# Kernel optimization log

Hardware: AMD Instinct MI355X
Metric: run time of the kernel (lower is better)

The kernel has to match this reference:

```python
import jax, jax.numpy as jnp
import numpy as np

B, S, D, DM, H = 2, 2048, 1024, 1024, 16
DH = D // H
EPS = 1e-5


def layernorm(x, g, b):
    m = jnp.mean(x, axis=-1, keepdims=True)
    v = jnp.mean(jnp.square(x - m), axis=-1, keepdims=True)
    return (x - m) * jax.lax.rsqrt(v + EPS) * g + b


def setup_inputs() -> dict:
    key = jax.random.key(0)
    ks = jax.random.split(key, 16)
    std = 0.02
    p = {
        'x': jax.random.normal(ks[0], (B, S, D), jnp.float32),
        'h': jnp.zeros((B, DM), jnp.float32),
        'c': jnp.zeros((B, DM), jnp.float32),
        'Wq': jax.random.normal(ks[1], (D, D), jnp.float32) * std,
        'Wk': jax.random.normal(ks[2], (D, D), jnp.float32) * std,
        'Wv': jax.random.normal(ks[3], (D, D), jnp.float32) * std,
        'Wo': jax.random.normal(ks[4], (D, D), jnp.float32) * std,
        'Wmk': jax.random.normal(ks[5], (DM, D), jnp.float32) * std,
        'Wmv': jax.random.normal(ks[6], (DM, D), jnp.float32) * std,
        'Wih': jax.random.normal(ks[7], (D, 4 * DM), jnp.float32) * std,
        'Whh': jax.random.normal(ks[8], (DM, 4 * DM), jnp.float32) * std,
        'b_ih': jnp.zeros((4 * DM,), jnp.float32),
        'b_hh': jnp.zeros((4 * DM,), jnp.float32),
        'W1': jax.random.normal(ks[9], (D, 4 * D), jnp.float32) * std,
        'bf1': jnp.zeros((4 * D,), jnp.float32),
        'W2': jax.random.normal(ks[10], (4 * D, D), jnp.float32) * std,
        'bf2': jnp.zeros((D,), jnp.float32),
        'g1': jnp.ones((D,), jnp.float32), 'be1': jnp.zeros((D,), jnp.float32),
        'g2': jnp.ones((D,), jnp.float32), 'be2': jnp.zeros((D,), jnp.float32),
        'g3': jnp.ones((D,), jnp.float32), 'be3': jnp.zeros((D,), jnp.float32),
        'Wmp': jax.random.normal(ks[11], (DM, D), jnp.float32) * std,
    }
    return p


def reference(x, h, c, Wq, Wk, Wv, Wo, Wmk, Wmv, Wih, Whh, b_ih, b_hh,
              W1, bf1, W2, bf2, g1, be1, g2, be2, g3, be3, Wmp):
    xn = layernorm(x, g1, be1)
    # projections, split heads: [B,S,D] -> [B,H,S,DH]
    def heads(t):
        return t.reshape(B, -1, H, DH).transpose(0, 2, 1, 3)
    Q = heads(xn @ Wq)
    Ks = heads(xn @ Wk)
    Vs = heads(xn @ Wv)
    Km = (h @ Wmk).reshape(B, 1, H, DH).transpose(0, 2, 1, 3)  # [B,H,1,DH]
    Vm = (h @ Wmv).reshape(B, 1, H, DH).transpose(0, 2, 1, 3)
    K = jnp.concatenate([Km, Ks], axis=2)  # [B,H,S+1,DH]
    V = jnp.concatenate([Vm, Vs], axis=2)
    scores = jnp.einsum('bhqd,bhkd->bhqk', Q, K) / jnp.sqrt(jnp.float32(DH))
    attn = jax.nn.softmax(scores, axis=-1)
    ao = jnp.einsum('bhqk,bhkd->bhqd', attn, V)
    ao = ao.transpose(0, 2, 1, 3).reshape(B, S, D)
    attended = x + ao @ Wo
    # LSTM step on mean-pooled tokens (torch LSTMCell gate order: i,f,g,o)
    pooled = jnp.mean(attended, axis=1)  # [B,D]
    gates = pooled @ Wih + b_ih + h @ Whh + b_hh
    i, f, g, o = jnp.split(gates, 4, axis=-1)
    new_c = jax.nn.sigmoid(f) * c + jax.nn.sigmoid(i) * jnp.tanh(g)
    new_h = jax.nn.sigmoid(o) * jnp.tanh(new_c)
    mixed = attended + (new_h @ Wmp)[:, None, :]
    hn = layernorm(mixed, g2, be2)
    ffn = jax.nn.gelu(hn @ W1 + bf1, approximate=False) @ W2 + bf2
    out = layernorm(mixed + ffn, g3, be3)
    return (out, new_h, new_c)
```

## Files before the change

kernel.cpp:

```cpp
#include <hip/hip_runtime.h>
#include <hip/hip_bf16.h>
#include <math.h>

#define BB 2
#define SS 2048
#define DD 1024
#define HH 16
#define RR (BB*SS)
#define KSTRIDE 2064
#define MB (1024ull*1024ull)

typedef unsigned short u16;
typedef unsigned int u32;
typedef __attribute__((ext_vector_type(8))) short short8v;
typedef __attribute__((ext_vector_type(4))) float f32x4;
typedef __attribute__((ext_vector_type(16))) float f32x16;
typedef __attribute__((ext_vector_type(4))) u16 u16x4;

__device__ __forceinline__ u16 f2bf(float f){
    union { __hip_bfloat16 h; u16 u; } c; c.h = __float2bfloat16(f); return c.u;
}
__device__ __forceinline__ u32 pk2(float a, float b){
    return (u32)f2bf(a) | ((u32)f2bf(b) << 16);
}
__device__ __forceinline__ float exp2_raw(float x){
    float r;
    asm("v_exp_f32 %0, %1" : "=v"(r) : "v"(x));
    return r;
}
__device__ __forceinline__ float erf_fast(float x){
    float ax = fabsf(x);
    float t = __builtin_amdgcn_rcpf(1.0f + 0.3275911f*ax);
    float y = t*(0.254829592f + t*(-0.284496736f + t*(1.421413741f + t*(-1.453152027f + t*1.061405429f))));
    float r = 1.0f - y*__expf(-ax*ax);
    return copysignf(r, x);
}

#define GLL16(gp, lp) __builtin_amdgcn_global_load_lds( \
    (const __attribute__((address_space(1))) void*)(gp), \
    (__attribute__((address_space(3))) void*)(lp), 16, 0, 0)

#define VMCNT8 asm volatile("s_waitcnt vmcnt(8)" ::: "memory")
#define VMCNT4 asm volatile("s_waitcnt vmcnt(4)" ::: "memory")
#define VMCNT0 asm volatile("s_waitcnt vmcnt(0)" ::: "memory")
#define SBAR   __builtin_amdgcn_s_barrier()
#define SCHEDB __builtin_amdgcn_sched_barrier(0)

__global__ __launch_bounds__(256) void ln_kernel(const float* __restrict__ in,
    const float* __restrict__ mproj, const float* __restrict__ g, const float* __restrict__ be,
    float* __restrict__ mixed_out, float* __restrict__ outf, u16* __restrict__ outb)
{
    int row = blockIdx.x; int b = row / SS; int tid = threadIdx.x;
    float4 v = ((const float4*)(in + (size_t)row*DD))[tid];
    if (mproj){
        float4 mp = ((const float4*)(mproj + (size_t)b*DD))[tid];
        v.x+=mp.x; v.y+=mp.y; v.z+=mp.z; v.w+=mp.w;
        ((float4*)(mixed_out + (size_t)row*DD))[tid] = v;
    }
    float s = v.x+v.y+v.z+v.w, s2 = v.x*v.x+v.y*v.y+v.z*v.z+v.w*v.w;
    #pragma unroll
    for (int off=32; off>0; off>>=1){ s += __shfl_down(s,off); s2 += __shfl_down(s2,off); }
    __shared__ float red[2][4];
    if ((tid&63)==0){ red[0][tid>>6]=s; red[1][tid>>6]=s2; }
    __syncthreads();
    float st = red[0][0]+red[0][1]+red[0][2]+red[0][3];
    float s2t= red[1][0]+red[1][1]+red[1][2]+red[1][3];
    float mean = st*(1.f/DD); float var = s2t*(1.f/DD)-mean*mean;
    float rs = rsqrtf(var + 1e-5f);
    float4 gg=((const float4*)g)[tid], bb2=((const float4*)be)[tid];
    float o0=(v.x-mean)*rs*gg.x+bb2.x, o1=(v.y-mean)*rs*gg.y+bb2.y;
    float o2=(v.z-mean)*rs*gg.z+bb2.z, o3=(v.w-mean)*rs*gg.w+bb2.w;
    if (outf){ float4 o={o0,o1,o2,o3}; ((float4*)(outf+(size_t)row*DD))[tid]=o; }
    if (outb){ u16x4 o={f2bf(o0),f2bf(o1),f2bf(o2),f2bf(o3)}; ((u16x4*)(outb+(size_t)row*DD))[tid]=o; }
}

__global__ __launch_bounds__(256) void ln3f_kernel(const float* __restrict__ p0,
    const float* __restrict__ p1a, const float* __restrict__ p1b,
    const float* __restrict__ bias, const float* __restrict__ resid,
    const float* __restrict__ g, const float* __restrict__ be, float* __restrict__ out)
{
    int row = blockIdx.x; int tid = threadIdx.x;
    const float* p1 = (row < 2048) ? (p1a + (size_t)row*DD) : (p1b + (size_t)(row-2048)*DD);
    float4 a  = ((const float4*)(p0 + (size_t)row*DD))[tid];
    float4 b  = ((const float4*)p1)[tid];
    float4 bi = ((const float4*)bias)[tid];
    float4 rs4= ((const float4*)(resid + (size_t)row*DD))[tid];
    float4 v = {a.x+b.x+bi.x+rs4.x, a.y+b.y+bi.y+rs4.y, a.z+b.z+bi.z+rs4.z, a.w+b.w+bi.w+rs4.w};
    float s = v.x+v.y+v.z+v.w, s2 = v.x*v.x+v.y*v.y+v.z*v.z+v.w*v.w;
    #pragma unroll
    for (int off=32; off>0; off>>=1){ s += __shfl_down(s,off); s2 += __shfl_down(s2,off); }
    __shared__ float red[2][4];
    if ((tid&63)==0){ red[0][tid>>6]=s; red[1][tid>>6]=s2; }
    __syncthreads();
    float st = red[0][0]+red[0][1]+red[0][2]+red[0][3];
    float s2t= red[1][0]+red[1][1]+red[1][2]+red[1][3];
    float mean = st*(1.f/DD); float var = s2t*(1.f/DD)-mean*mean;
    float rs = rsqrtf(var + 1e-5f);
    float4 gg=((const float4*)g)[tid], bb2=((const float4*)be)[tid];
    float4 o;
    o.x=(v.x-mean)*rs*gg.x+bb2.x; o.y=(v.y-mean)*rs*gg.y+bb2.y;
    o.z=(v.z-mean)*rs*gg.z+bb2.z; o.w=(v.w-mean)*rs*gg.w+bb2.w;
    ((float4*)(out + (size_t)row*DD))[tid] = o;
}

__global__ __launch_bounds__(256) void tr6_kernel(const float* __restrict__ Wq, const float* __restrict__ Wk,
    const float* __restrict__ Wv, const float* __restrict__ Wo,
    const float* __restrict__ W1, const float* __restrict__ W2,
    u16* __restrict__ WqkvT, u16* __restrict__ WoT, u16* __restrict__ W1T, u16* __restrict__ W2T)
{
    __shared__ float t[32][33];
    int bid = blockIdx.x;
    const float* in; u16* out; int K, N, n0, k0;
    if (bid < 3072){
        int m = bid >> 10, r = bid & 1023;
        in = (m==0) ? Wq : (m==1) ? Wk : Wv;
        out = WqkvT + (size_t)m*1024*1024;
        K = 1024; N = 1024; n0 = (r & 31)*32; k0 = (r >> 5)*32;
    } else if (bid < 4096){
        int r = bid - 3072;
        in = Wo; out = WoT; K = 1024; N = 1024; n0 = (r & 31)*32; k0 = (r >> 5)*32;
    } else if (bid < 8192){
        int r = bid - 4096;
        in = W1; out = W1T; K = 1024; N = 4096; n0 = (r & 127)*32; k0 = (r >> 7)*32;
    } else {
        int r = bid - 8192;
        in = W2; out = W2T; K = 4096; N = 1024; n0 = (r & 31)*32; k0 = (r >> 5)*32;
    }
    int tx = threadIdx.x & 31, ty = threadIdx.x >> 5;
    #pragma unroll
    for (int i=0;i<4;i++){ int k = ty + i*8; t[k][tx] = in[(size_t)(k0+k)*N + n0 + tx]; }
    __syncthreads();
    #pragma unroll
    for (int i=0;i<4;i++){ int n = ty + i*8; out[(size_t)(n0+n)*K + k0 + tx] = f2bf(t[tx][n]); }
}

__global__ __launch_bounds__(512) void mgemm256(const u16* __restrict__ A, const u16* __restrict__ BT,
    int nbx, int K, int mode, const float* __restrict__ bias, float scale,
    void* __restrict__ Cout, void* __restrict__ C2a, void* __restrict__ C2b)
{
    __shared__ __align__(16) u16 lds[2][2][2][256*32];
    int tid = threadIdx.x, l = tid&63, w = tid>>6;
    int wr = w>>2, wc = w&3;
    int nwg = gridDim.x, q8 = nwg>>3;
    int bid = blockIdx.x;
    int swz = (bid & 7)*q8 + (bid >> 3);
    int by = swz / nbx, bx = swz % nbx;
    int bm = by*256, bn = bx*256;
    const int NT = K >> 6;

    f32x4 acc[8][4];
    #pragma unroll
    for (int i=0;i<8;i++)
        #pragma unroll
        for (int j=0;j<4;j++)
            #pragma unroll
            for (int r=0;r<4;r++) acc[i][j][r]=0.f;

    auto stage_plane = [&](int buf, int op, int ks, int tt){
        const u16* base = op ? BT : A;
        int tile0 = op ? bn : bm;
        #pragma unroll
        for (int i=0;i<2;i++){
            int rbase = (w*2+i)*16;
            int row = rbase + (l>>2);
            int slotlog = (l&3) ^ ((row>>1)&3);
            const u16* g = base + (size_t)(tile0 + row)*K + tt*64 + ks*32 + slotlog*8;
            GLL16(g, (u16*)&lds[buf][op][ks][0] + rbase*32);
        }
    };
    auto ds_a = [&](int buf, int ks, int ai) -> short8v {
        int row = wr*128 + ai*16 + (l&15);
        int slot = (l>>4) ^ ((row>>1)&3);
        return *(const short8v*)((const char*)&lds[buf][0][ks][0] + row*64 + slot*16);
    };
    auto ds_b = [&](int buf, int ks, int bi) -> short8v {
        int row = wc*64 + bi*16 + (l&15);
        int slot = (l>>4) ^ ((row>>1)&3);
        return *(const short8v*)((const char*)&lds[buf][1][ks][0] + row*64 + slot*16);
    };

    stage_plane(0,0,0,0); stage_plane(0,1,0,0);
    stage_plane(0,0,1,0); stage_plane(0,1,1,0);
    stage_plane(1,0,0,1); stage_plane(1,1,0,1);
    VMCNT8;
    SBAR; SCHEDB;

    for (int t=0; t<NT; t++){
        int buf = t&1, obuf = buf^1;
        bool s1 = (t+1 < NT), s2 = (t+2 < NT);
        short8v b0,b1,b2,b3, a0,a1,a2,a3;
        b0=ds_b(buf,0,0); b1=ds_b(buf,0,1); b2=ds_b(buf,0,2); b3=ds_b(buf,0,3);
        a0=ds_a(buf,0,0); a1=ds_a(buf,0,1); a2=ds_a(buf,0,2); a3=ds_a(buf,0,3);
        if (s1) stage_plane(obuf,0,1,t+1);
        __builtin_amdgcn_s_setprio(1);
        acc[0][0]=__builtin_amdgcn_mfma_f32_16x16x32_bf16(b0,a0,acc[0][0],0,0,0);
        acc[0][1]=__builtin_amdgcn_mfma_f32_16x16x32_bf16(b1,a0,acc[0][1],0,0,0);
        acc[0][2]=__builtin_amdgcn_mfma_f32_16x16x32_bf16(b2,a0,acc[0][2],0,0,0);
        acc[0][3]=__builtin_amdgcn_mfma_f32_16x16x32_bf16(b3,a0,acc[0][3],0,0,0);
        acc[1][0]=__builtin_amdgcn_mfma_f32_16x16x32_bf16(b0,a1,acc[1][0],0,0,0);
        acc[1][1]=__builtin_amdgcn_mfma_f32_16x16x32_bf16(b1,a1,acc[1][1],0,0,0);
        acc[1][2]=__builtin_amdgcn_mfma_f32_16x16x32_bf16(b2,a1,acc[1][2],0,0,0);
        acc[1][3]=__builtin_amdgcn_mfma_f32_16x16x32_bf16(b3,a1,acc[1][3],0,0,0);
        acc[2][0]=__builtin_amdgcn_mfma_f32_16x16x32_bf16(b0,a2,acc[2][0],0,0,0);
        acc[2][1]=__builtin_amdgcn_mfma_f32_16x16x32_bf16(b1,a2,acc[2][1],0,0,0);
        acc[2][2]=__builtin_amdgcn_mfma_f32_16x16x32_bf16(b2,a2,acc[2][2],0,0,0);
        acc[2][3]=__builtin_amdgcn_mfma_f32_16x16x32_bf16(b3,a2,acc[2][3],0,0,0);
        acc[3][0]=__builtin_amdgcn_mfma_f32_16x16x32_bf16(b0,a3,acc[3][0],0,0,0);
        acc[3][1]=__builtin_amdgcn_mfma_f32_16x16x32_bf16(b1,a3,acc[3][1],0,0,0);
        acc[3][2]=__builtin_amdgcn_mfma_f32_16x16x32_bf16(b2,a3,acc[3][2],0,0,0);
        acc[3][3]=__builtin_amdgcn_mfma_f32_16x16x32_bf16(b3,a3,acc[3][3],0,0,0);
        __builtin_amdgcn_s_setprio(0);
        SBAR; SCHEDB;
        a0=ds_a(buf,0,4); a1=ds_a(buf,0,5); a2=ds_a(buf,0,6); a3=ds_a(buf,0,7);
        if (s1) stage_plane(obuf,1,1,t+1);
        __builtin_amdgcn_s_setprio(1);
        acc[4][0]=__builtin_amdgcn_mfma_f32_16x16x32_bf16(b0,a0,acc[4][0],0,0,0);
        acc[4][1]=__builtin_amdgcn_mfma_f32_16x16x32_bf16(b1,a0,acc[4][1],0,0,0);
        acc[4][2]=__builtin_amdgcn_mfma_f32_16x16x32_bf16(b2,a0,acc[4][2],0,0,0);
        acc[4][3]=__builtin_amdgcn_mfma_f32_16x16x32_bf16(b3,a0,acc[4][3],0,0,0);
        acc[5][0]=__builtin_amdgcn_mfma_f32_16x16x32_bf16(b0,a1,acc[5][0],0,0,0);
        acc[5][1]=__builtin_amdgcn_mfma_f32_16x16x32_bf16(b1,a1,acc[5][1],0,0,0);
        acc[5][2]=__builtin_amdgcn_mfma_f32_16x16x32_bf16(b2,a1,acc[5][2],0,0,0);
        acc[5][3]=__builtin_amdgcn_mfma_f32_16x16x32_bf16(b3,a1,acc[5][3],0,0,0);
        acc[6][0]=__builtin_amdgcn_mfma_f32_16x16x32_bf16(b0,a2,acc[6][0],0,0,0);
        acc[6][1]=__builtin_amdgcn_mfma_f32_16x16x32_bf16(b1,a2,acc[6][1],0,0,0);
        acc[6][2]=__builtin_amdgcn_mfma_f32_16x16x32_bf16(b2,a2,acc[6][2],0,0,0);
        acc[6][3]=__builtin_amdgcn_mfma_f32_16x16x32_bf16(b3,a2,acc[6][3],0,0,0);
        acc[7][0]=__builtin_amdgcn_mfma_f32_16x16x32_bf16(b0,a3,acc[7][0],0,0,0);
        acc[7][1]=__builtin_amdgcn_mfma_f32_16x16x32_bf16(b1,a3,acc[7][1],0,0,0);
        acc[7][2]=__builtin_amdgcn_mfma_f32_16x16x32_bf16(b2,a3,acc[7][2],0,0,0);
        acc[7][3]=__builtin_amdgcn_mfma_f32_16x16x32_bf16(b3,a3,acc[7][3],0,0,0);
        __builtin_amdgcn_s_setprio(0);
        if (s1) { VMCNT8; } else { VMCNT0; }
        SBAR; SCHEDB;
        b0=ds_b(buf,1,0); b1=ds_b(buf,1,1); b2=ds_b(buf,1,2); b3=ds_b(buf,1,3);
        a0=ds_a(buf,1,0); a1=ds_a(buf,1,1); a2=ds_a(buf,1,2); a3=ds_a(buf,1,3);
        if (s2) stage_plane(buf,0,0,t+2);
        __builtin_amdgcn_s_setprio(1);
        acc[0][0]=__builtin_amdgcn_mfma_f32_16x16x32_bf16(b0,a0,acc[0][0],0,0,0);
        acc[0][1]=__builtin_amdgcn_mfma_f32_16x16x32_bf16(b1,a0,acc[0][1],0,0,0);
        acc[0][2]=__builtin_amdgcn_mfma_f32_16x16x32_bf16(b2,a0,acc[0][2],0,0,0);
        acc[0][3]=__builtin_amdgcn_mfma_f32_16x16x32_bf16(b3,a0,acc[0][3],0,0,0);
        acc[1][0]=__builtin_amdgcn_mfma_f32_16x16x32_bf16(b0,a1,acc[1][0],0,0,0);
        acc[1][1]=__builtin_amdgcn_mfma_f32_16x16x32_bf16(b1,a1,acc[1][1],0,0,0);
        acc[1][2]=__builtin_amdgcn_mfma_f32_16x16x32_bf16(b2,a1,acc[1][2],0,0,0);
        acc[1][3]=__builtin_amdgcn_mfma_f32_16x16x32_bf16(b3,a1,acc[1][3],0,0,0);
        acc[2][0]=__builtin_amdgcn_mfma_f32_16x16x32_bf16(b0,a2,acc[2][0],0,0,0);
        acc[2][1]=__builtin_amdgcn_mfma_f32_16x16x32_bf16(b1,a2,acc[2][1],0,0,0);
        acc[2][2]=__builtin_amdgcn_mfma_f32_16x16x32_bf16(b2,a2,acc[2][2],0,0,0);
        acc[2][3]=__builtin_amdgcn_mfma_f32_16x16x32_bf16(b3,a2,acc[2][3],0,0,0);
        acc[3][0]=__builtin_amdgcn_mfma_f32_16x16x32_bf16(b0,a3,acc[3][0],0,0,0);
        acc[3][1]=__builtin_amdgcn_mfma_f32_16x16x32_bf16(b1,a3,acc[3][1],0,0,0);
        acc[3][2]=__builtin_amdgcn_mfma_f32_16x16x32_bf16(b2,a3,acc[3][2],0,0,0);
        acc[3][3]=__builtin_amdgcn_mfma_f32_16x16x32_bf16(b3,a3,acc[3][3],0,0,0);
        __builtin_amdgcn_s_setprio(0);
        SBAR; SCHEDB;
        a0=ds_a(buf,1,4); a1=ds_a(buf,1,5); a2=ds_a(buf,1,6); a3=ds_a(buf,1,7);
        if (s2) stage_plane(buf,1,0,t+2);
        __builtin_amdgcn_s_setprio(1);
        acc[4][0]=__builtin_amdgcn_mfma_f32_16x16x32_bf16(b0,a0,acc[4][0],0,0,0);
        acc[4][1]=__builtin_amdgcn_mfma_f32_16x16x32_bf16(b1,a0,acc[4][1],0,0,0);
        acc[4][2]=__builtin_amdgcn_mfma_f32_16x16x32_bf16(b2,a0,acc[4][2],0,0,0);
        acc[4][3]=__builtin_amdgcn_mfma_f32_16x16x32_bf16(b3,a0,acc[4][3],0,0,0);
        acc[5][0]=__builtin_amdgcn_mfma_f32_16x16x32_bf16(b0,a1,acc[5][0],0,0,0);
        acc[5][1]=__builtin_amdgcn_mfma_f32_16x16x32_bf16(b1,a1,acc[5][1],0,0,0);
        acc[5][2]=__builtin_amdgcn_mfma_f32_16x16x32_bf16(b2,a1,acc[5][2],0,0,0);
        acc[5][3]=__builtin_amdgcn_mfma_f32_16x16x32_bf16(b3,a1,acc[5][3],0,0,0);
        acc[6][0]=__builtin_amdgcn_mfma_f32_16x16x32_bf16(b0,a2,acc[6][0],0,0,0);
        acc[6][1]=__builtin_amdgcn_mfma_f32_16x16x32_bf16(b1,a2,acc[6][1],0,0,0);
        acc[6][2]=__builtin_amdgcn_mfma_f32_16x16x32_bf16(b2,a2,acc[6][2],0,0,0);
        acc[6][3]=__builtin_amdgcn_mfma_f32_16x16x32_bf16(b3,a2,acc[6][3],0,0,0);
        acc[7][0]=__builtin_amdgcn_mfma_f32_16x16x32_bf16(b0,a3,acc[7][0],0,0,0);
        acc[7][1]=__builtin_amdgcn_mfma_f32_16x16x32_bf16(b1,a3,acc[7][1],0,0,0);
        acc[7][2]=__builtin_amdgcn_mfma_f32_16x16x32_bf16(b2,a3,acc[7][2],0,0,0);
        acc[7][3]=__builtin_amdgcn_mfma_f32_16x16x32_bf16(b3,a3,acc[7][3],0,0,0);
        __builtin_amdgcn_s_setprio(0);
        if (s2) { VMCNT8; } else if (s1) { VMCNT4; } else { VMCNT0; }
        SBAR; SCHEDB;
    }

    #pragma unroll
    for (int ai=0; ai<8; ai++){
        int m = bm + wr*128 + ai*16 + (l&15);
        #pragma unroll
        for (int bi=0; bi<4; bi++){
            int nb = bn + wc*64 + bi*16 + ((l>>4)<<2);
            f32x4 v = acc[ai][bi];
            if (mode == 0){
                float4 bv = *(const float4*)(bias + nb);
                float t0=v[0]+bv.x, t1=v[1]+bv.y, t2=v[2]+bv.z, t3=v[3]+bv.w;
                u16x4 o;
                o[0]=f2bf(0.5f*t0*(1.0f+erf_fast(t0*0.70710678118654752f)));
                o[1]=f2bf(0.5f*t1*(1.0f+erf_fast(t1*0.70710678118654752f)));
                o[2]=f2bf(0.5f*t2*(1.0f+erf_fast(t2*0.70710678118654752f)));
                o[3]=f2bf(0.5f*t3*(1.0f+erf_fast(t3*0.70710678118654752f)));
                *(u16x4*)((u16*)Cout + (size_t)m*(nbx*256) + nb) = o;
            } else {
                if (nb < 1024){
                    u16x4 o;
                    #pragma unroll
                    for (int r=0;r<4;r++) o[r] = f2bf(v[r]*scale);
                    *(u16x4*)((u16*)Cout + (size_t)m*1024 + nb) = o;
                } else if (nb < 2048){
                    int cc = nb-1024; int hh = cc>>6, dh = cc&63;
                    int b2 = m>>11, key = m&2047;
                    u16x4 o;
                    #pragma unroll
                    for (int r=0;r<4;r++) o[r] = f2bf(v[r]);
                    *(u16x4*)((u16*)C2a + ((size_t)(b2*HH+hh)*KSTRIDE + key)*64 + dh) = o;
                } else {
                    int cc = nb-2048; int hh = cc>>6, dh = cc&63;
                    int b2 = m>>11, key = m&2047;
                    #pragma unroll
                    for (int r=0;r<4;r++)
                        ((u16*)C2b)[((size_t)(b2*HH+hh)*64 + dh + r)*KSTRIDE + key] = f2bf(v[r]);
                }
            }
        }
    }
}

#define MODE_F32R 3
#define MODE_PART 6

__global__ __launch_bounds__(256) void mgemm(const u16* __restrict__ A, const u16* __restrict__ BT,
    int nbx, int Kc, int kchunks, int mode,
    const float* __restrict__ bias, const float* __restrict__ resid, float scale,
    void* __restrict__ Cout, void* __restrict__ C2a, void* __restrict__ C2b)
{
    int tid=threadIdx.x, l=tid&63, w=tid>>6;
    int nwg = gridDim.x;
    int qq = nwg >> 3;
    int bid = blockIdx.x;
    int swz = (bid & 7)*qq + (bid >> 3);
    int tiles = nwg / kchunks;
    int chunk = swz / tiles;
    int t2 = swz % tiles;
    int sby = t2 / (nbx*8);
    int rem = t2 - sby*(nbx*8);
    int sbx = rem >> 6;
    int ci  = rem & 63;
    int bx = sbx*8 + (ci&7);
    int by = sby*8 + (ci>>3);

    int bm = by*128, bn = bx*128;
    int N = nbx*128;
    int lda = Kc*kchunks;
    int koff = chunk*Kc;
    int wr = w>>1, wc = w&1;
    f32x4 acc[4][4];
    #pragma unroll
    for(int i=0;i<4;i++)
        #pragma unroll
        for(int j=0;j<4;j++)
            #pragma unroll
            for(int r=0;r<4;r++) acc[i][j][r]=0.f;

    __shared__ __align__(16) u16 Al[2][4096];
    __shared__ __align__(16) u16 Bl[2][4096];
    int srow = (w<<4) + (l>>2);
    int sph  = l&3;
    const int NT = Kc >> 5;

    auto stage = [&](int buf, int kt){
        #pragma unroll
        for (int r=0;r<2;r++){
            int rowA = srow + r*64;
            int sl = sph ^ ((rowA>>1)&3);
            const u16* gA = A + (size_t)(bm+rowA)*lda + koff + kt*32 + sl*8;
            GLL16(gA, (char*)&Al[buf][0] + r*4096 + w*1024);
            const u16* gB = BT + (size_t)(bn+rowA)*lda + koff + kt*32 + sl*8;
            GLL16(gB, (char*)&Bl[buf][0] + r*4096 + w*1024);
        }
    };

    int cur=0;
    stage(0,0);
    __syncthreads();
    for (int kt=0; kt<NT; kt++){
        if (kt+1<NT) stage(cur^1, kt+1);
        short8v af[4], bf[4];
        #pragma unroll
        for (int mi=0;mi<4;mi++){
            int row = wr*64 + mi*16 + (l&15);
            int sl = (l>>4) ^ ((row>>1)&3);
            af[mi] = *(const short8v*)((const char*)&Al[cur][0] + row*64 + sl*16);
        }
        #pragma unroll
        for (int ni=0;ni<4;ni++){
            int row = wc*64 + ni*16 + (l&15);
            int sl = (l>>4) ^ ((row>>1)&3);
            bf[ni] = *(const short8v*)((const char*)&Bl[cur][0] + row*64 + sl*16);
        }
        #pragma unroll
        for (int mi=0;mi<4;mi++)
            #pragma unroll
            for (int ni=0;ni<4;ni++)
                acc[mi][ni] = __builtin_amdgcn_mfma_f32_16x16x32_bf16(bf[ni], af[mi], acc[mi][ni], 0,0,0);
        __syncthreads();
        cur ^= 1;
    }

    #pragma unroll
    for (int mi=0;mi<4;mi++){
        int m = bm + wr*64 + mi*16 + (l&15);
        #pragma unroll
        for (int ni=0;ni<4;ni++){
            int nb = bn + wc*64 + ni*16 + ((l>>4)<<2);
            f32x4 v = acc[mi][ni];
            if (mode==MODE_F32R){
                float4 rs = *(const float4*)(resid + (size_t)m*N + nb);
                float4 o = {v[0]+rs.x, v[1]+rs.y, v[2]+rs.z, v[3]+rs.w};
                *(float4*)((float*)Cout + (size_t)m*N + nb) = o;
            } else {
                float4 o = {v[0],v[1],v[2],v[3]};
                if (chunk==0)       *(float4*)((float*)Cout + (size_t)m*N + nb) = o;
                else if (m < 2048)  *(float4*)((float*)C2a  + (size_t)m*N + nb) = o;
                else                *(float4*)((float*)C2b  + (size_t)(m-2048)*N + nb) = o;
            }
        }
    }
}

__global__ __launch_bounds__(256) void attn_mfma(const u16* __restrict__ Qb, const u16* __restrict__ Kb,
    const u16* __restrict__ VTb, u16* __restrict__ ao)
{
    __shared__ __align__(16) u16 Kl[3][4096];
    __shared__ __align__(16) u16 Vl[3][4096];
    int tid=threadIdx.x, l=tid&63, w=tid>>6;
    int l31=l&31, hi=l>>5;
    int bid = blockIdx.x;
    int xcd = bid & 7, idx = bid >> 3;
    int bh = xcd*4 + (idx>>4);
    int qt = idx & 15;
    int b=bh>>4, h=bh&15;
    int qrow = qt*128 + w*32 + l31;

    const u16* qptr = Qb + (size_t)(b*SS + qrow)*DD + h*64;
    short8v qf[4];
    #pragma unroll
    for (int t=0;t<4;t++) qf[t] = *(const short8v*)(qptr + t*16 + hi*8);

    f32x16 so0, so1;
    #pragma unroll
    for (int i=0;i<16;i++){ so0[i]=0.f; so1[i]=0.f; }
    float l_run=0.f;

    int skey = (w<<3) + (l>>3);
    int ssl  = l&7;
    auto stage = [&](int buf, int kt){
        #pragma unroll
        for (int r=0;r<2;r++){
            int key = skey + r*32;
            int slot = ssl ^ (key&7);
            const u16* gK = Kb + ((size_t)bh*KSTRIDE + kt*64 + key)*64 + slot*8;
            GLL16(gK, (char*)&Kl[buf][0] + r*4096 + w*1024);
            const u16* gV = VTb + ((size_t)bh*64 + key)*KSTRIDE + kt*64 + slot*8;
            GLL16(gV, (char*)&Vl[buf][0] + r*4096 + w*1024);
        }
    };

    auto QK = [&](int bf, f32x16& s0, f32x16& s1){
        #pragma unroll
        for (int i=0;i<16;i++){ s0[i]=0.f; s1[i]=0.f; }
        __builtin_amdgcn_s_setprio(1);
        #pragma unroll
        for (int t=0;t<4;t++){
            int sl = (2*t+hi) ^ (l31&7);
            short8v kf0 = *(const short8v*)((const char*)&Kl[bf][0] + l31*128 + sl*16);
            s0 = __builtin_amdgcn_mfma_f32_32x32x16_bf16(kf0, qf[t], s0, 0,0,0);
            short8v kf1 = *(const short8v*)((const char*)&Kl[bf][0] + (32+l31)*128 + sl*16);
            s1 = __builtin_amdgcn_mfma_f32_32x32x16_bf16(kf1, qf[t], s1, 0,0,0);
        }
        __builtin_amdgcn_s_setprio(0);
    };

    auto SMPV = [&](int bf, f32x16& s0, f32x16& s1){
        float psum = 0.f;
        #pragma unroll
        for (int r=0;r<16;r++){
            float p=exp2_raw(s0[r]); s0[r]=p; psum+=p;
            float q=exp2_raw(s1[r]); s1[r]=q; psum+=q;
        }
        psum += __shfl_xor(psum, 32);
        l_run += psum;
        short8v pf[4];
        #pragma unroll
        for (int t=0;t<4;t++){
            u32 a0,a1,b0,b1;
            if (t==0){ a0=pk2(s0[0],s0[1]);   a1=pk2(s0[2],s0[3]);   b0=pk2(s0[4],s0[5]);   b1=pk2(s0[6],s0[7]); }
            else if (t==1){ a0=pk2(s0[8],s0[9]);   a1=pk2(s0[10],s0[11]); b0=pk2(s0[12],s0[13]); b1=pk2(s0[14],s0[15]); }
            else if (t==2){ a0=pk2(s1[0],s1[1]);   a1=pk2(s1[2],s1[3]);   b0=pk2(s1[4],s1[5]);   b1=pk2(s1[6],s1[7]); }
            else          { a0=pk2(s1[8],s1[9]);   a1=pk2(s1[10],s1[11]); b0=pk2(s1[12],s1[13]); b1=pk2(s1[14],s1[15]); }
            u32 sx0 = hi ? a0 : b0, sx1 = hi ? a1 : b1;
            u32 r0 = (u32)__shfl_xor((int)sx0, 32);
            u32 r1 = (u32)__shfl_xor((int)sx1, 32);
            union { u32 u[4]; short8v v; } cvt;
            cvt.u[0] = hi ? r0 : a0;
            cvt.u[1] = hi ? r1 : a1;
            cvt.u[2] = hi ? b0 : r0;
            cvt.u[3] = hi ? b1 : r1;
            pf[t] = cvt.v;
        }
        __builtin_amdgcn_s_setprio(1);
        #pragma unroll
        for (int t=0;t<4;t++){
            int sl = (2*t+hi) ^ (l31&7);
            short8v vf0 = *(const short8v*)((const char*)&Vl[bf][0] + l31*128 + sl*16);
            so0 = __builtin_amdgcn_mfma_f32_32x32x16_bf16(vf0, pf[t], so0, 0,0,0);
            short8v vf1 = *(const short8v*)((const char*)&Vl[bf][0] + (32+l31)*128 + sl*16);
            so1 = __builtin_amdgcn_mfma_f32_32x32x16_bf16(vf1, pf[t], so1, 0,0,0);
        }
        __builtin_amdgcn_s_setprio(0);
    };

    const int NTILE = 33;
    int bufA = 0, bufB = 1, bufC = 2;
    stage(0, 0);
    stage(1, 1);
    __syncthreads();

    f32x16 sA0, sA1, sB0, sB1;
    QK(bufA, sA0, sA1);

    auto ITER = [&](f32x16& c0, f32x16& c1, f32x16& n0, f32x16& n1, int t){
        if (t+2 < NTILE) stage(bufC, t+2);
        QK(bufB, n0, n1);
        SMPV(bufA, c0, c1);
        __syncthreads();
        int tmp = bufA; bufA = bufB; bufB = bufC; bufC = tmp;
    };
    #pragma unroll 1
    for (int tt=0; tt<16; tt++){
        ITER(sA0, sA1, sB0, sB1, 2*tt);
        ITER(sB0, sB1, sA0, sA1, 2*tt+1);
    }
    #pragma unroll
    for (int r=0;r<16;r++){
        int k0 = 2048 + (r&3) + 8*(r>>2) + 4*hi;
        if (k0 >= 2049) sA0[r] = -1e30f;
        sA1[r] = -1e30f;
    }
    SMPV(bufA, sA0, sA1);

    float inv = 1.f / l_run;
    u16* aop = ao + (size_t)(b*SS + qrow)*DD + h*64;
    #pragma unroll
    for (int rg=0; rg<4; rg++){
        int dh0 = rg*8 + 4*hi;
        u16x4 o0, o1;
        #pragma unroll
        for (int j=0;j<4;j++){ o0[j]=f2bf(so0[rg*4+j]*inv); o1[j]=f2bf(so1[rg*4+j]*inv); }
        *(u16x4*)(aop + dh0) = o0;
        *(u16x4*)(aop + 32 + dh0) = o1;
    }
}

__global__ __launch_bounds__(256) void vecmat_part(const float* __restrict__ vec,
    const float* __restrict__ W, float* __restrict__ part, int K, int N)
{
    int b = blockIdx.z, kc = blockIdx.y;
    int j = blockIdx.x*256 + threadIdx.x;
    int k0 = kc * (K >> 3);
    float acc = 0.0f;
    #pragma unroll 4
    for (int k = k0; k < k0 + (K >> 3); k++)
        acc += vec[(size_t)b*K + k] * W[(size_t)k*N + j];
    part[((size_t)b*8 + kc)*N + j] = acc;
}

__global__ __launch_bounds__(256) void vecmat_red(const float* __restrict__ part,
    float* __restrict__ out, int N)
{
    int b = blockIdx.y;
    int j = blockIdx.x*256 + threadIdx.x;
    float acc = 0.0f;
    #pragma unroll
    for (int kc = 0; kc < 8; kc++) acc += part[((size_t)b*8 + kc)*N + j];
    out[(size_t)b*N + j] = acc;
}

__global__ __launch_bounds__(256) void vecmat2_part(const float* __restrict__ vec,
    const float* __restrict__ Wa, const float* __restrict__ Wb, float* __restrict__ part)
{
    int b = blockIdx.z, kc = blockIdx.y;
    int j = blockIdx.x*256 + threadIdx.x;
    int k0 = kc * 128;
    float accA = 0.0f, accB = 0.0f;
    #pragma unroll 4
    for (int k = k0; k < k0 + 128; k++){
        float v = vec[(size_t)b*DD + k];
        accA += v * Wa[(size_t)k*DD + j];
        accB += v * Wb[(size_t)k*DD + j];
    }
    part[((size_t)b*8 + kc)*2048 + j] = accA;
    part[((size_t)b*8 + kc)*2048 + 1024 + j] = accB;
}

__global__ __launch_bounds__(256) void vecmat2_red(const float* __restrict__ part,
    float* __restrict__ outA, float* __restrict__ outB)
{
    int b = blockIdx.y;
    int j = blockIdx.x*256 + threadIdx.x;
    float accA = 0.0f, accB = 0.0f;
    #pragma unroll
    for (int kc = 0; kc < 8; kc++){
        accA += part[((size_t)b*8 + kc)*2048 + j];
        accB += part[((size_t)b*8 + kc)*2048 + 1024 + j];
    }
    outA[(size_t)b*DD + j] = accA;
    outB[(size_t)b*DD + j] = accB;
}

__global__ __launch_bounds__(256) void fixup_kernel(const float* __restrict__ Kmb,
    const float* __restrict__ Vmb, u16* __restrict__ Kb, u16* __restrict__ VTb)
{
    int idx = blockIdx.x*256 + threadIdx.x;
    int b = idx>>10, j = idx&1023; int h=j>>6, dh=j&63; int bh=b*HH+h;
    Kb[((size_t)bh*KSTRIDE + 2048)*64 + dh] = f2bf(Kmb[idx]);
    VTb[((size_t)bh*64 + dh)*KSTRIDE + 2048] = f2bf(Vmb[idx]);
}

__global__ __launch_bounds__(256) void pool1_kernel(const float* __restrict__ att, float* __restrict__ ppart)
{
    int b = blockIdx.y, sc = blockIdx.x;
    int tid = threadIdx.x;
    float4 acc = {0,0,0,0};
    for (int s = 0; s < 32; s++) {
        int row = b*SS + sc*32 + s;
        float4 v = ((const float4*)(att + (size_t)row*DD))[tid];
        acc.x += v.x; acc.y += v.y; acc.z += v.z; acc.w += v.w;
    }
    ((float4*)(ppart + ((size_t)b*64 + sc)*DD))[tid] = acc;
}

__global__ __launch_bounds__(256) void pool2_kernel(const float* __restrict__ ppart, float* __restrict__ pooled)
{
    int b = blockIdx.y;
    int j = blockIdx.x*256 + threadIdx.x;
    float acc = 0.0f;
    for (int sc = 0; sc < 64; sc++) acc += ppart[((size_t)b*64 + sc)*DD + j];
    pooled[(size_t)b*DD + j] = acc * (1.0f/SS);
}

__global__ __launch_bounds__(256) void gates_part(const float* __restrict__ pooled,
    const float* __restrict__ h, const float* __restrict__ Wih, const float* __restrict__ Whh,
    float* __restrict__ part)
{
    int b = blockIdx.z, kc = blockIdx.y;
    int j = blockIdx.x*256 + threadIdx.x;
    int k0 = kc * 64;
    float acc = 0.0f;
    #pragma unroll 4
    for (int k = k0; k < k0 + 64; k++)
        acc += pooled[(size_t)b*DD + k] * Wih[(size_t)k*4*DD + j]
             + h[(size_t)b*DD + k]      * Whh[(size_t)k*4*DD + j];
    part[((size_t)b*16 + kc)*4*DD + j] = acc;
}

__device__ __forceinline__ float sigmoidf_(float x) { return 1.0f / (1.0f + __expf(-x)); }

__global__ __launch_bounds__(256) void lstm_kernel(const float* __restrict__ gpart,
    const float* __restrict__ b_ih, const float* __restrict__ b_hh,
    const float* __restrict__ c, float* __restrict__ newh_ws, float* __restrict__ out_tail)
{
    int idx = blockIdx.x*256 + threadIdx.x;
    int b = idx >> 10, d = idx & 1023;
    float sI = b_ih[d]          + b_hh[d];
    float sF = b_ih[DD + d]     + b_hh[DD + d];
    float sG = b_ih[2*DD + d]   + b_hh[2*DD + d];
    float sO = b_ih[3*DD + d]   + b_hh[3*DD + d];
    #pragma unroll
    for (int kc = 0; kc < 16; kc++){
        const float* gp = gpart + ((size_t)b*16 + kc)*4*DD;
        sI += gp[d]; sF += gp[DD + d]; sG += gp[2*DD + d]; sO += gp[3*DD + d];
    }
    float ig = sigmoidf_(sI);
    float fg = sigmoidf_(sF);
    float gg = tanhf(sG);
    float og = sigmoidf_(sO);
    float nc = fg * c[idx] + ig * gg;
    float nh = og * tanhf(nc);
    newh_ws[idx] = nh;
    out_tail[idx] = nh;
    out_tail[BB*DD + idx] = nc;
}

extern "C" void kernel_launch(void* const* d_in, const int* in_sizes, int n_in,
                              void* d_out, int out_size, void* d_ws, size_t ws_size,
                              hipStream_t stream) {
    const float* x    = (const float*)d_in[0];
    const float* h    = (const float*)d_in[1];
    const float* c    = (const float*)d_in[2];
    const float* Wq   = (const float*)d_in[3];
    const float* Wk   = (const float*)d_in[4];
    const float* Wv   = (const float*)d_in[5];
    const float* Wo   = (const float*)d_in[6];
    const float* Wmk  = (const float*)d_in[7];
    const float* Wmv  = (const float*)d_in[8];
    const float* Wih  = (const float*)d_in[9];
    const float* Whh  = (const float*)d_in[10];
    const float* b_ih = (const float*)d_in[11];
    const float* b_hh = (const float*)d_in[12];
    const float* W1   = (const float*)d_in[13];
    const float* bf1  = (const float*)d_in[14];
    const float* W2   = (const float*)d_in[15];
    const float* bf2  = (const float*)d_in[16];
    const float* g1   = (const float*)d_in[17];
    const float* be1  = (const float*)d_in[18];
    const float* g2   = (const float*)d_in[19];
    const float* be2  = (const float*)d_in[20];
    const float* g3   = (const float*)d_in[21];
    const float* be3  = (const float*)d_in[22];
    const float* Wmp  = (const float*)d_in[23];

    float* out = (float*)d_out;
    char* wsb  = (char*)d_ws;

    u16*   xn   = (u16*)(wsb + 0);
    u16*   hn   = (u16*)(wsb + 8*MB);
    float* p0   = (float*)(wsb + 0);
    u16*   Qbuf = (u16*)(wsb + 16*MB);
    u16*   Kbuf = (u16*)(wsb + 24*MB);
    u16*   VTb  = (u16*)(wsb + 33*MB);
    u16*   act  = (u16*)(wsb + 16*MB);
    u16*   ao   = (u16*)(wsb + 48*MB);
    float* p1a  = (float*)(wsb + 48*MB);
    float* attb = (float*)(wsb + 56*MB);
    u16*   WqkvT= (u16*)(wsb + 72*MB);
    u16*   WoT  = (u16*)(wsb + 78*MB);
    u16*   W1T  = (u16*)(wsb + 80*MB);
    float* p1b  = (float*)(wsb + 80*MB);
    u16*   W2T  = (u16*)(wsb + 88*MB);
    float* sm   = (float*)(wsb + 96*MB);
    float* Kmb     = sm;
    float* Vmb     = Kmb + 2048;
    float* pooled  = Vmb + 2048;
    float* newh    = pooled + 2048;
    float* mproj   = newh + 2048;
    float* vpart   = mproj + 2048;
    float* v2part  = vpart + 16384;
    float* gpart   = v2part + 32768;
    float* ppart   = gpart + 131072;

    tr6_kernel<<<12288, 256, 0, stream>>>(Wq, Wk, Wv, Wo, W1, W2, WqkvT, WoT, W1T, W2T);

    ln_kernel<<<RR, 256, 0, stream>>>(x, nullptr, g1, be1, nullptr, nullptr, xn);
    vecmat2_part<<<dim3(4,8,BB), 256, 0, stream>>>(h, Wmk, Wmv, v2part);
    vecmat2_red<<<dim3(4,BB), 256, 0, stream>>>(v2part, Kmb, Vmb);
    mgemm256<<<192, 512, 0, stream>>>(xn, WqkvT, 12, 1024, 1, nullptr,
                                      0.125f*1.44269504088896f, Qbuf, Kbuf, VTb);
    fixup_kernel<<<8, 256, 0, stream>>>(Kmb, Vmb, Kbuf, VTb);
    attn_mfma<<<512, 256, 0, stream>>>(Qbuf, Kbuf, VTb, ao);
    mgemm<<<8*32, 256, 0, stream>>>(ao, WoT, 8, 1024, 1, MODE_F32R, nullptr, x, 1.f, attb, nullptr, nullptr);
    pool1_kernel<<<dim3(64,BB), 256, 0, stream>>>(attb, ppart);
    pool2_kernel<<<dim3(4,BB), 256, 0, stream>>>(ppart, pooled);
    gates_part<<<dim3(16,16,BB), 256, 0, stream>>>(pooled, h, Wih, Whh, gpart);
    lstm_kernel<<<8, 256, 0, stream>>>(gpart, b_ih, b_hh, c, newh, out + (size_t)RR*DD);
    vecmat_part<<<dim3(4,8,BB), 256, 0, stream>>>(newh, Wmp, vpart, DD, DD);
    vecmat_red<<<dim3(4,BB), 256, 0, stream>>>(vpart, mproj, DD);
    ln_kernel<<<RR, 256, 0, stream>>>(attb, mproj, g2, be2, attb, nullptr, hn);
    mgemm256<<<256, 512, 0, stream>>>(hn, W1T, 16, 1024, 0, bf1, 1.f, act, nullptr, nullptr);
    mgemm<<<8*32*2, 256, 0, stream>>>(act, W2T, 8, 2048, 2, MODE_PART, nullptr, nullptr, 1.f, p0, p1a, p1b);
    ln3f_kernel<<<RR, 256, 0, stream>>>(p0, p1a, p1b, bf2, attb, g3, be3, out);
}
```

Before: 303.9 us.

## Run W2 GEMM on 256-tile kernel with 4-way split-K bf16 partials

The FFN down-projection moves from the 128-tile mgemm with 2-way split-K fp32 partials to the 256x256-tile mgemm256 with 4-way split-K. Each partial is written as bf16, and the final layernorm kernel sums the four bf16 partials. The attention kernel now packs probabilities with v_cvt_pk_bf16_f32 and, when the builtin is available, exchanges halves with permlane32_swap instead of shuffles. These aim to cut partial-sum memory traffic and GEMM tiling overhead, at the cost of extra rounding error from bf16 partials.

```diff
diff --git a/kernel.cpp b/kernel.cpp
--- a/kernel.cpp
+++ b/kernel.cpp
@@ -20,13 +20,18 @@
 __device__ __forceinline__ u16 f2bf(float f){
     union { __hip_bfloat16 h; u16 u; } c; c.h = __float2bfloat16(f); return c.u;
 }
-__device__ __forceinline__ u32 pk2(float a, float b){
-    return (u32)f2bf(a) | ((u32)f2bf(b) << 16);
+__device__ __forceinline__ u32 cvtpk(float a, float b){
+    u32 r;
+    asm("v_cvt_pk_bf16_f32 %0, %1, %2" : "=v"(r) : "v"(a), "v"(b));
+    return r;
 }
 __device__ __forceinline__ float exp2_raw(float x){
     float r;
     asm("v_exp_f32 %0, %1" : "=v"(r) : "v"(x));
     return r;
+}
+__device__ __forceinline__ float bf2f(u16 u){
+    union { u32 i; float f; } c; c.i = (u32)u << 16; return c.f;
 }
 __device__ __forceinline__ float erf_fast(float x){
     float ax = fabsf(x);
@@ -74,21 +79,27 @@
     if (outb){ u16x4 o={f2bf(o0),f2bf(o1),f2bf(o2),f2bf(o3)}; ((u16x4*)(outb+(size_t)row*DD))[tid]=o; }
 }
 
-__global__ __launch_bounds__(256) void ln3f_kernel(const float* __restrict__ p0,
-    const float* __restrict__ p1a, const float* __restrict__ p1b,
+__global__ __launch_bounds__(256) void ln3f_kernel(const u16* __restrict__ pb0,
+    const u16* __restrict__ pb1, const u16* __restrict__ pb2, const u16* __restrict__ pb3,
     const float* __restrict__ bias, const float* __restrict__ resid,
     const float* __restrict__ g, const float* __restrict__ be, float* __restrict__ out)
 {
     int row = blockIdx.x; int tid = threadIdx.x;
-    const float* p1 = (row < 2048) ? (p1a + (size_t)row*DD) : (p1b + (size_t)(row-2048)*DD);
-    float4 a  = ((const float4*)(p0 + (size_t)row*DD))[tid];
-    float4 b  = ((const float4*)p1)[tid];
+    size_t off = (size_t)row*DD;
+    u16x4 q0 = ((const u16x4*)(pb0+off))[tid];
+    u16x4 q1 = ((const u16x4*)(pb1+off))[tid];
+    u16x4 q2 = ((const u16x4*)(pb2+off))[tid];
+    u16x4 q3 = ((const u16x4*)(pb3+off))[tid];
     float4 bi = ((const float4*)bias)[tid];
-    float4 rs4= ((const float4*)(resid + (size_t)row*DD))[tid];
-    float4 v = {a.x+b.x+bi.x+rs4.x, a.y+b.y+bi.y+rs4.y, a.z+b.z+bi.z+rs4.z, a.w+b.w+bi.w+rs4.w};
+    float4 rs4= ((const float4*)(resid+off))[tid];
+    float4 v;
+    v.x = bf2f(q0[0])+bf2f(q1[0])+bf2f(q2[0])+bf2f(q3[0]) + bi.x + rs4.x;
+    v.y = bf2f(q0[1])+bf2f(q1[1])+bf2f(q2[1])+bf2f(q3[1]) + bi.y + rs4.y;
+    v.z = bf2f(q0[2])+bf2f(q1[2])+bf2f(q2[2])+bf2f(q3[2]) + bi.z + rs4.z;
+    v.w = bf2f(q0[3])+bf2f(q1[3])+bf2f(q2[3])+bf2f(q3[3]) + bi.w + rs4.w;
     float s = v.x+v.y+v.z+v.w, s2 = v.x*v.x+v.y*v.y+v.z*v.z+v.w*v.w;
     #pragma unroll
-    for (int off=32; off>0; off>>=1){ s += __shfl_down(s,off); s2 += __shfl_down(s2,off); }
+    for (int off2=32; off2>0; off2>>=1){ s += __shfl_down(s,off2); s2 += __shfl_down(s2,off2); }
     __shared__ float red[2][4];
     if ((tid&63)==0){ red[0][tid>>6]=s; red[1][tid>>6]=s2; }
     __syncthreads();
@@ -100,7 +111,7 @@
     float4 o;
     o.x=(v.x-mean)*rs*gg.x+bb2.x; o.y=(v.y-mean)*rs*gg.y+bb2.y;
     o.z=(v.z-mean)*rs*gg.z+bb2.z; o.w=(v.w-mean)*rs*gg.w+bb2.w;
-    ((float4*)(out + (size_t)row*DD))[tid] = o;
+    ((float4*)(out + off))[tid] = o;
 }
 
 __global__ __launch_bounds__(256) void tr6_kernel(const float* __restrict__ Wq, const float* __restrict__ Wk,
@@ -135,8 +146,8 @@
 }
 
 __global__ __launch_bounds__(512) void mgemm256(const u16* __restrict__ A, const u16* __restrict__ BT,
-    int nbx, int K, int mode, const float* __restrict__ bias, float scale,
-    void* __restrict__ Cout, void* __restrict__ C2a, void* __restrict__ C2b)
+    int nbx, int Kc, int kchunks, int mode, const float* __restrict__ bias, float scale,
+    void* __restrict__ Cout, void* __restrict__ C2a, void* __restrict__ C2b, void* __restrict__ C2c)
 {
     __shared__ __align__(16) u16 lds[2][2][2][256*32];
     int tid = threadIdx.x, l = tid&63, w = tid>>6;
@@ -144,9 +155,14 @@
     int nwg = gridDim.x, q8 = nwg>>3;
     int bid = blockIdx.x;
     int swz = (bid & 7)*q8 + (bid >> 3);
-    int by = swz / nbx, bx = swz % nbx;
+    int tiles = nwg / kchunks;
+    int chunk = swz / tiles;
+    int t2 = swz % tiles;
+    int by = t2 / nbx, bx = t2 % nbx;
     int bm = by*256, bn = bx*256;
-    const int NT = K >> 6;
+    int lda = Kc*kchunks;
+    int koff = chunk*Kc;
+    const int NT = Kc >> 6;
 
     f32x4 acc[8][4];
     #pragma unroll
@@ -164,7 +180,7 @@
             int rbase = (w*2+i)*16;
             int row = rbase + (l>>2);
             int slotlog = (l&3) ^ ((row>>1)&3);
-            const u16* g = base + (size_t)(tile0 + row)*K + tt*64 + ks*32 + slotlog*8;
+            const u16* g = base + (size_t)(tile0 + row)*lda + koff + tt*64 + ks*32 + slotlog*8;
             GLL16(g, (u16*)&lds[buf][op][ks][0] + rbase*32);
         }
     };
@@ -279,6 +295,7 @@
         SBAR; SCHEDB;
     }
 
+    int N = nbx*256;
     #pragma unroll
     for (int ai=0; ai<8; ai++){
         int m = bm + wr*128 + ai*16 + (l&15);
@@ -294,8 +311,8 @@
                 o[1]=f2bf(0.5f*t1*(1.0f+erf_fast(t1*0.70710678118654752f)));
                 o[2]=f2bf(0.5f*t2*(1.0f+erf_fast(t2*0.70710678118654752f)));
                 o[3]=f2bf(0.5f*t3*(1.0f+erf_fast(t3*0.70710678118654752f)));
-                *(u16x4*)((u16*)Cout + (size_t)m*(nbx*256) + nb) = o;
-            } else {
+                *(u16x4*)((u16*)Cout + (size_t)m*N + nb) = o;
+            } else if (mode == 1){
                 if (nb < 1024){
                     u16x4 o;
                     #pragma unroll
@@ -315,13 +332,19 @@
                     for (int r=0;r<4;r++)
                         ((u16*)C2b)[((size_t)(b2*HH+hh)*64 + dh + r)*KSTRIDE + key] = f2bf(v[r]);
                 }
+            } else {
+                u16* pp = (chunk==0) ? (u16*)Cout : (chunk==1) ? (u16*)C2a :
+                          (chunk==2) ? (u16*)C2b : (u16*)C2c;
+                u16x4 o;
+                #pragma unroll
+                for (int r=0;r<4;r++) o[r] = f2bf(v[r]);
+                *(u16x4*)(pp + (size_t)m*N + nb) = o;
             }
         }
     }
 }
 
 #define MODE_F32R 3
-#define MODE_PART 6
 
 __global__ __launch_bounds__(256) void mgemm(const u16* __restrict__ A, const u16* __restrict__ BT,
     int nbx, int Kc, int kchunks, int mode,
@@ -408,16 +431,9 @@
         for (int ni=0;ni<4;ni++){
             int nb = bn + wc*64 + ni*16 + ((l>>4)<<2);
             f32x4 v = acc[mi][ni];
-            if (mode==MODE_F32R){
-                float4 rs = *(const float4*)(resid + (size_t)m*N + nb);
-                float4 o = {v[0]+rs.x, v[1]+rs.y, v[2]+rs.z, v[3]+rs.w};
-                *(float4*)((float*)Cout + (size_t)m*N + nb) = o;
-            } else {
-                float4 o = {v[0],v[1],v[2],v[3]};
-                if (chunk==0)       *(float4*)((float*)Cout + (size_t)m*N + nb) = o;
-                else if (m < 2048)  *(float4*)((float*)C2a  + (size_t)m*N + nb) = o;
-                else                *(float4*)((float*)C2b  + (size_t)(m-2048)*N + nb) = o;
-            }
+            float4 rs = *(const float4*)(resid + (size_t)m*N + nb);
+            float4 o = {v[0]+rs.x, v[1]+rs.y, v[2]+rs.z, v[3]+rs.w};
+            *(float4*)((float*)Cout + (size_t)m*N + nb) = o;
         }
     }
 }
@@ -488,18 +504,27 @@
         #pragma unroll
         for (int t=0;t<4;t++){
             u32 a0,a1,b0,b1;
-            if (t==0){ a0=pk2(s0[0],s0[1]);   a1=pk2(s0[2],s0[3]);   b0=pk2(s0[4],s0[5]);   b1=pk2(s0[6],s0[7]); }
-            else if (t==1){ a0=pk2(s0[8],s0[9]);   a1=pk2(s0[10],s0[11]); b0=pk2(s0[12],s0[13]); b1=pk2(s0[14],s0[15]); }
-            else if (t==2){ a0=pk2(s1[0],s1[1]);   a1=pk2(s1[2],s1[3]);   b0=pk2(s1[4],s1[5]);   b1=pk2(s1[6],s1[7]); }
-            else          { a0=pk2(s1[8],s1[9]);   a1=pk2(s1[10],s1[11]); b0=pk2(s1[12],s1[13]); b1=pk2(s1[14],s1[15]); }
+            if (t==0){ a0=cvtpk(s0[0],s0[1]);   a1=cvtpk(s0[2],s0[3]);   b0=cvtpk(s0[4],s0[5]);   b1=cvtpk(s0[6],s0[7]); }
+            else if (t==1){ a0=cvtpk(s0[8],s0[9]);   a1=cvtpk(s0[10],s0[11]); b0=cvtpk(s0[12],s0[13]); b1=cvtpk(s0[14],s0[15]); }
+            else if (t==2){ a0=cvtpk(s1[0],s1[1]);   a1=cvtpk(s1[2],s1[3]);   b0=cvtpk(s1[4],s1[5]);   b1=cvtpk(s1[6],s1[7]); }
+            else          { a0=cvtpk(s1[8],s1[9]);   a1=cvtpk(s1[10],s1[11]); b0=cvtpk(s1[12],s1[13]); b1=cvtpk(s1[14],s1[15]); }
+            union { u32 u[4]; short8v v; } cvt;
+#if __has_builtin(__builtin_amdgcn_permlane32_swap)
+            auto r0 = __builtin_amdgcn_permlane32_swap(a0, b0, false, false);
+            auto r1 = __builtin_amdgcn_permlane32_swap(a1, b1, false, false);
+            cvt.u[0] = (u32)r0[0];
+            cvt.u[1] = (u32)r1[0];
+            cvt.u[2] = (u32)r0[1];
+            cvt.u[3] = (u32)r1[1];
+#else
             u32 sx0 = hi ? a0 : b0, sx1 = hi ? a1 : b1;
             u32 r0 = (u32)__shfl_xor((int)sx0, 32);
             u32 r1 = (u32)__shfl_xor((int)sx1, 32);
-            union { u32 u[4]; short8v v; } cvt;
             cvt.u[0] = hi ? r0 : a0;
             cvt.u[1] = hi ? r1 : a1;
             cvt.u[2] = hi ? b0 : r0;
             cvt.u[3] = hi ? b1 : r1;
+#endif
             pf[t] = cvt.v;
         }
         __builtin_amdgcn_s_setprio(1);
@@ -719,18 +744,19 @@
 
     u16*   xn   = (u16*)(wsb + 0);
     u16*   hn   = (u16*)(wsb + 8*MB);
-    float* p0   = (float*)(wsb + 0);
+    u16*   pb0  = (u16*)(wsb + 0);
+    u16*   pb1  = (u16*)(wsb + 8*MB);
     u16*   Qbuf = (u16*)(wsb + 16*MB);
     u16*   Kbuf = (u16*)(wsb + 24*MB);
     u16*   VTb  = (u16*)(wsb + 33*MB);
     u16*   act  = (u16*)(wsb + 16*MB);
     u16*   ao   = (u16*)(wsb + 48*MB);
-    float* p1a  = (float*)(wsb + 48*MB);
+    u16*   pb2  = (u16*)(wsb + 48*MB);
     float* attb = (float*)(wsb + 56*MB);
     u16*   WqkvT= (u16*)(wsb + 72*MB);
     u16*   WoT  = (u16*)(wsb + 78*MB);
     u16*   W1T  = (u16*)(wsb + 80*MB);
-    float* p1b  = (float*)(wsb + 80*MB);
+    u16*   pb3  = (u16*)(wsb + 80*MB);
     u16*   W2T  = (u16*)(wsb + 88*MB);
     float* sm   = (float*)(wsb + 96*MB);
     float* Kmb     = sm;
@@ -748,8 +774,8 @@
     ln_kernel<<<RR, 256, 0, stream>>>(x, nullptr, g1, be1, nullptr, nullptr, xn);
     vecmat2_part<<<dim3(4,8,BB), 256, 0, stream>>>(h, Wmk, Wmv, v2part);
     vecmat2_red<<<dim3(4,BB), 256, 0, stream>>>(v2part, Kmb, Vmb);
-    mgemm256<<<192, 512, 0, stream>>>(xn, WqkvT, 12, 1024, 1, nullptr,
-                                      0.125f*1.44269504088896f, Qbuf, Kbuf, VTb);
+    mgemm256<<<192, 512, 0, stream>>>(xn, WqkvT, 12, 1024, 1, 1, nullptr,
+                                      0.125f*1.44269504088896f, Qbuf, Kbuf, VTb, nullptr);
     fixup_kernel<<<8, 256, 0, stream>>>(Kmb, Vmb, Kbuf, VTb);
     attn_mfma<<<512, 256, 0, stream>>>(Qbuf, Kbuf, VTb, ao);
     mgemm<<<8*32, 256, 0, stream>>>(ao, WoT, 8, 1024, 1, MODE_F32R, nullptr, x, 1.f, attb, nullptr, nullptr);
@@ -760,7 +786,7 @@
     vecmat_part<<<dim3(4,8,BB), 256, 0, stream>>>(newh, Wmp, vpart, DD, DD);
     vecmat_red<<<dim3(4,BB), 256, 0, stream>>>(vpart, mproj, DD);
     ln_kernel<<<RR, 256, 0, stream>>>(attb, mproj, g2, be2, attb, nullptr, hn);
-    mgemm256<<<256, 512, 0, stream>>>(hn, W1T, 16, 1024, 0, bf1, 1.f, act, nullptr, nullptr);
-    mgemm<<<8*32*2, 256, 0, stream>>>(act, W2T, 8, 2048, 2, MODE_PART, nullptr, nullptr, 1.f, p0, p1a, p1b);
-    ln3f_kernel<<<RR, 256, 0, stream>>>(p0, p1a, p1b, bf2, attb, g3, be3, out);
-}
+    mgemm256<<<256, 512, 0, stream>>>(hn, W1T, 16, 1024, 1, 0, bf1, 1.f, act, nullptr, nullptr, nullptr);
+    mgemm256<<<256, 512, 0, stream>>>(act, W2T, 4, 1024, 4, 2, nullptr, 1.f, pb0, pb1, pb2, pb3);
+    ln3f_kernel<<<RR, 256, 0, stream>>>(pb0, pb1, pb2, pb3, bf2, attb, g3, be3, out);
+}
```

Result: faster. 291.0 us (-4.3%).
